# Kernel tuning notes

Measured on AMD Instinct MI355X. Metric: run time of the kernel, lower is better.

Reference implementation:

```python
import jax, jax.numpy as jnp
import numpy as np
import math

EMBED_DIMS = 256
NUM_LANDMARKS = 40  # hard-coded k=40 in the original module
B, N = 2, 8192


def setup_inputs() -> dict:
    key = jax.random.key(0)
    ks = jax.random.split(key, 9)
    C = EMBED_DIMS
    w = lambda k: jax.random.normal(k, (C, C), dtype=jnp.float32) * 0.02
    b = lambda k: jax.random.normal(k, (C,), dtype=jnp.float32) * 0.02
    return {
        "query": jax.random.normal(ks[0], (B, N, C), dtype=jnp.float32),
        "Wq": w(ks[1]), "bq": b(ks[2]),
        "Wk": w(ks[3]), "bk": b(ks[4]),
        "Wv": w(ks[5]), "bv": b(ks[6]),
        "Wo": w(ks[7]), "bo": b(ks[8]),
    }


def reference(query, Wq, bq, Wk, bk, Wv, bv, Wo, bo):
    # key = value = identity = query (defaults in the original forward)
    C = query.shape[-1]
    scaling = math.sqrt(C)

    q = query @ Wq.T + bq  # [B, N, C]
    k = query @ Wk.T + bk
    v = query @ Wv.T + bv

    # Full similarity only to score keys: score_m[b, m] = sum_n sim_nm[b, n, m]
    sim_nm = jnp.einsum('bnc,bmc->bnm', q, k) / scaling  # [B, N, N]
    score_m = sim_nm.sum(axis=1)                          # [B, N]

    _, top_idx = jax.lax.top_k(score_m, NUM_LANDMARKS)    # [B, 40]
    selected = jnp.take_along_axis(k, top_idx[:, :, None], axis=1)  # [B, 40, C]

    sim_qn = jax.nn.softmax(jnp.einsum('bnc,bkc->bnk', q, selected) / scaling, axis=-1)  # [B, N, 40]
    sim_km = jax.nn.softmax(jnp.einsum('bmc,bkc->bmk', k, selected) / scaling, axis=-1)  # [B, N, 40]

    sim_qk = jnp.einsum('bnk,bmk->bnm', sim_qn, sim_km)   # [B, N, N]
    out = jnp.einsum('bnm,bmc->bnc', sim_qk, v)           # [B, N, C]
    out = out @ Wo.T + bo
    return query + out  # identity residual; dropouts are identity at p=0
```

## Files before the change

### kernel.cpp

```cpp
#include <hip/hip_runtime.h>
#include <cstddef>
#include <cstdint>

#define BATCH 2
#define SEQ 8192
#define CH 256
#define NLM 40
#define MROWS (BATCH * SEQ)
#define INV_SCALE 0.0625f
#define NCBLK 256

typedef unsigned short ushort_t;
typedef __attribute__((ext_vector_type(8))) short short8;
typedef __attribute__((ext_vector_type(4))) float floatx4;

__device__ __forceinline__ ushort_t f2bf(float f) {
    unsigned int u = __float_as_uint(f);
    u += 0x7FFFu + ((u >> 16) & 1u);
    return (ushort_t)(u >> 16);
}
__device__ __forceinline__ float bf2f(ushort_t u) {
    return __uint_as_float(((unsigned)u) << 16);
}

__global__ __launch_bounds__(256) void convert_colsum(const float* __restrict__ x,
                                                      ushort_t* __restrict__ xbf,
                                                      float* __restrict__ partial) {
    __shared__ float red[4][256];
    const int b = blockIdx.y;
    const int r0 = blockIdx.x * 32;
    const int t = threadIdx.x;
    const int c4 = (t & 63) * 4;
    const int rg = t >> 6;
    const float* base = x + ((size_t)b * SEQ + r0) * 256;
    ushort_t* obase = xbf + ((size_t)b * SEQ + r0) * 256;
    float4 s = {0.f, 0.f, 0.f, 0.f};
#pragma unroll
    for (int i = 0; i < 8; i++) {
        const int r = rg + i * 4;
        const float4 a = *(const float4*)&base[(size_t)r * 256 + c4];
        uint2 o;
        o.x = f2bf(a.x) | ((unsigned)f2bf(a.y) << 16);
        o.y = f2bf(a.z) | ((unsigned)f2bf(a.w) << 16);
        *(uint2*)&obase[(size_t)r * 256 + c4] = o;
        s.x += a.x; s.y += a.y; s.z += a.z; s.w += a.w;
    }
    *(float4*)&red[rg][c4] = s;
    __syncthreads();
    const float tot = red[0][t] + red[1][t] + red[2][t] + red[3][t];
    partial[((size_t)b * NCBLK + blockIdx.x) * 256 + t] = tot;
}

__global__ __launch_bounds__(1024) void ws_kernel(const float* __restrict__ partial,
                                                  const float* __restrict__ Wq,
                                                  const float* __restrict__ bq,
                                                  const float* __restrict__ Wk,
                                                  float* __restrict__ ws,
                                                  float* __restrict__ tmat) {
    const int b = blockIdx.x;
    __shared__ float xs[256];
    __shared__ float qs[256];
    __shared__ float ppart[4][256];
    const int t = threadIdx.x;
    {
        float* tz = tmat + (size_t)b * NLM * 256;
        for (int i = t; i < NLM * 256; i += 1024) tz[i] = 0.f;
    }
    {
        const int c = t & 255, qd = t >> 8;
        const float* pb = partial + ((size_t)b * NCBLK + qd * 64) * 256 + c;
        float a = 0.f;
#pragma unroll 8
        for (int i = 0; i < 64; i++) a += pb[(size_t)i * 256];
        ppart[qd][c] = a;
    }
    __syncthreads();
    if (t < 256) xs[t] = ppart[0][t] + ppart[1][t] + ppart[2][t] + ppart[3][t];
    __syncthreads();
    const int lane = t & 63, w = t >> 6;
    for (int g = 0; g < 16; g++) {
        const int o = w * 16 + g;
        const float4 wq = *(const float4*)&Wq[(size_t)o * 256 + lane * 4];
        const float4 x4 = *(const float4*)&xs[lane * 4];
        float d = wq.x * x4.x + wq.y * x4.y + wq.z * x4.z + wq.w * x4.w;
#pragma unroll
        for (int off = 32; off >= 1; off >>= 1) d += __shfl_down(d, off);
        if (lane == 0) qs[o] = d + 8192.0f * bq[o];
    }
    __syncthreads();
    const int c = t & 255, part = t >> 8;
    float a = 0.f;
    for (int o = part * 64; o < part * 64 + 64; o++)
        a += Wk[(size_t)o * 256 + c] * qs[o];
    ppart[part][c] = a;
    __syncthreads();
    if (t < 256)
        ws[b * 256 + t] = ppart[0][t] + ppart[1][t] + ppart[2][t] + ppart[3][t];
}

__global__ __launch_bounds__(256) void gemm_qkv_score(const ushort_t* __restrict__ xbf,
                                                      const float* __restrict__ Wq,
                                                      const float* __restrict__ Wk,
                                                      const float* __restrict__ Wv,
                                                      const float* __restrict__ bq,
                                                      const float* __restrict__ bk,
                                                      const float* __restrict__ bv,
                                                      ushort_t* __restrict__ qkv,
                                                      const float* __restrict__ query,
                                                      const float* __restrict__ ws,
                                                      float* __restrict__ score) {
    __shared__ __align__(16) ushort_t As[128 * 72];
    __shared__ __align__(16) ushort_t Bs[64 * 40];
    const int z = blockIdx.z;
    const int t = threadIdx.x;
    const int lane = t & 63;
    const int w = t >> 6;

    if (z == 3) {
        const int blk = blockIdx.y * 4 + blockIdx.x;
#pragma unroll
        for (int i = 0; i < 8; i++) {
            const int g = blk * 32 + i * 4 + w;
            const int b = g >> 13;
            const int m = g & 8191;
            const float4 kv = *(const float4*)&query[(size_t)g * 256 + lane * 4];
            const float4 qs = *(const float4*)&ws[b * 256 + lane * 4];
            float d = kv.x * qs.x + kv.y * qs.y + kv.z * qs.z + kv.w * qs.w;
#pragma unroll
            for (int off = 32; off >= 1; off >>= 1) d += __shfl_down(d, off);
            if (lane == 0) score[(size_t)b * SEQ + m] = d * INV_SCALE;
        }
        return;
    }

    const float* __restrict__ W = (z == 0) ? Wq : (z == 1) ? Wk : Wv;
    const float* __restrict__ bias = (z == 0) ? bq : (z == 1) ? bk : bv;
    ushort_t* __restrict__ out = qkv + (size_t)z * MROWS * 256;
    const int o0 = blockIdx.x * 64;
    const int m0 = blockIdx.y * 128;
    const int quad = lane >> 4;
    const int l16 = lane & 15;

    floatx4 acc[2][4];
#pragma unroll
    for (int rt = 0; rt < 2; rt++)
#pragma unroll
        for (int ct = 0; ct < 4; ct++) acc[rt][ct] = (floatx4){0.f, 0.f, 0.f, 0.f};

    for (int kc = 0; kc < 256; kc += 32) {
#pragma unroll
        for (int u = 0; u < 2; u++) {
            const int cid = t + u * 256;
            const int row = cid >> 2, off = cid & 3;
            *(uint4*)&As[row * 40 + off * 8] =
                *(const uint4*)&xbf[(size_t)(m0 + row) * 256 + kc + off * 8];
        }
        {
            const int row = t >> 2, off = t & 3;
            const float* wp = &W[(size_t)(o0 + row) * 256 + kc + off * 8];
            const float4 a = *(const float4*)wp;
            const float4 c = *(const float4*)(wp + 4);
            uint4 o;
            o.x = f2bf(a.x) | ((unsigned)f2bf(a.y) << 16);
            o.y = f2bf(a.z) | ((unsigned)f2bf(a.w) << 16);
            o.z = f2bf(c.x) | ((unsigned)f2bf(c.y) << 16);
            o.w = f2bf(c.z) | ((unsigned)f2bf(c.w) << 16);
            *(uint4*)&Bs[row * 40 + off * 8] = o;
        }
        __syncthreads();
        short8 a[2], b[4];
#pragma unroll
        for (int rt = 0; rt < 2; rt++)
            a[rt] = *(const short8*)&As[(w * 32 + rt * 16 + l16) * 40 + quad * 8];
#pragma unroll
        for (int ct = 0; ct < 4; ct++)
            b[ct] = *(const short8*)&Bs[(ct * 16 + l16) * 40 + quad * 8];
#pragma unroll
        for (int rt = 0; rt < 2; rt++)
#pragma unroll
            for (int ct = 0; ct < 4; ct++)
                acc[rt][ct] = __builtin_amdgcn_mfma_f32_16x16x32_bf16(
                    a[rt], b[ct], acc[rt][ct], 0, 0, 0);
        __syncthreads();
    }

#pragma unroll
    for (int rt = 0; rt < 2; rt++) {
#pragma unroll
        for (int ct = 0; ct < 4; ct++) {
            const int col = ct * 16 + l16;
            const float bb = bias[o0 + col];
#pragma unroll
            for (int reg = 0; reg < 4; reg++) {
                const int row = w * 32 + rt * 16 + quad * 4 + reg;
                As[row * 72 + col] = f2bf(acc[rt][ct][reg] + bb);
            }
        }
    }
    __syncthreads();
#pragma unroll
    for (int u = 0; u < 4; u++) {
        const int cid = t + u * 256;
        const int row = cid >> 3;
        const int off = (cid & 7) * 8;
        *(uint4*)&out[(size_t)(m0 + row) * 256 + o0 + off] =
            *(const uint4*)&As[row * 72 + off];
    }
}

__global__ __launch_bounds__(1024) void topk_gather(const float* __restrict__ score,
                                                    const ushort_t* __restrict__ kmat,
                                                    float* __restrict__ sel) {
    const int b = blockIdx.x;
    const int t = threadIdx.x;
    __shared__ unsigned hist[256];
    __shared__ unsigned wsum[64];
    __shared__ unsigned sPrefix, sMask, sRem, sNeq;
    __shared__ int sNgt;
    __shared__ int top[NLM];
    __shared__ unsigned topkey[NLM];

    unsigned key[8];
#pragma unroll
    for (int j = 0; j < 8; j++) {
        const unsigned u = __float_as_uint(score[(size_t)b * SEQ + t + j * 1024]);
        key[j] = u ^ (unsigned)(((int)u >> 31) | 0x80000000);
    }
    if (t == 0) { sPrefix = 0; sMask = 0; sRem = NLM; sNgt = 0; sNeq = 0; }

    for (int lvl = 0; lvl < 4; lvl++) {
        const int shift = 24 - 8 * lvl;
        if (t < 256) hist[t] = 0;
        __syncthreads();
        const unsigned pfx = sPrefix, msk = sMask;
#pragma unroll
        for (int j = 0; j < 8; j++)
            if (((key[j] ^ pfx) & msk) == 0)
                atomicAdd(&hist[(key[j] >> shift) & 255u], 1u);
        __syncthreads();
        if (t < 64) wsum[t] = hist[t * 4] + hist[t * 4 + 1] + hist[t * 4 + 2] + hist[t * 4 + 3];
        __syncthreads();
        if (t == 0) {
            unsigned rem = sRem, cum = 0;
            int g = 63;
            for (; g > 0; g--) { if (cum + wsum[g] >= rem) break; cum += wsum[g]; }
            int d = g * 4 + 3;
            for (; d > g * 4; d--) { if (cum + hist[d] >= rem) break; cum += hist[d]; }
            sRem = rem - cum;
            sPrefix |= ((unsigned)d) << shift;
            sMask |= 255u << shift;
        }
        __syncthreads();
    }
    const unsigned K40 = sPrefix;
    const unsigned rem = sRem;
    const int ngt = NLM - (int)rem;

#pragma unroll
    for (int j = 0; j < 8; j++) {
        if (key[j] > K40) {
            const int slot = atomicAdd(&sNgt, 1);
            top[slot] = t + j * 1024; topkey[slot] = key[j];
        } else if (key[j] == K40) {
            const unsigned e = atomicAdd(&sNeq, 1u);
            if (e < rem) {
                const int slot = ngt + (int)e;
                top[slot] = t + j * 1024; topkey[slot] = key[j];
            }
        }
    }
    __syncthreads();

    if (t < 64) {
        unsigned long long c = (t < NLM)
            ? ((((unsigned long long)(~topkey[t])) << 32) | (unsigned)top[t])
            : 0xFFFFFFFFFFFFFFFFull;
#pragma unroll
        for (int kk = 2; kk <= 64; kk <<= 1) {
#pragma unroll
            for (int j = kk >> 1; j >= 1; j >>= 1) {
                const unsigned long long o = __shfl_xor(c, j);
                const bool takeMin = ((t & kk) == 0) == ((t & j) == 0);
                const bool less = c < o;
                c = (takeMin == less) ? c : o;
            }
        }
        if (t < NLM) top[t] = (int)(c & 0xFFFFFFFFu);
    }
    __syncthreads();

    for (int f = t; f < NLM * 256; f += 1024) {
        const int j = f >> 8;
        const int cc = f & 255;
        sel[(size_t)b * SEQ * 0 + (size_t)b * NLM * 256 + f] = bf2f(kmat[((size_t)b * SEQ + top[j]) * 256 + cc]);
    }
}

__global__ __launch_bounds__(256, 4) void sim_fused(const ushort_t* __restrict__ qbf,
                                                    const ushort_t* __restrict__ kbf,
                                                    const ushort_t* __restrict__ vbf,
                                                    const float* __restrict__ sel,
                                                    float* __restrict__ simq,
                                                    float* __restrict__ tmat) {
    __shared__ __align__(16) char smem[43008];
    float (*As_)[68] = (float(*)[68])smem;
    float (*St_)[68] = (float(*)[68])(smem + 17408);
    float (*Ps)[40]  = (float(*)[40])smem;
    ushort_t* Vs     = (ushort_t*)(smem + 10240);
    const int b = blockIdx.y;
    const int n0 = blockIdx.x * 64;
    const int t = threadIdx.x;
    const int r = t >> 2, c = t & 3;
    const ushort_t* __restrict__ A = (blockIdx.z == 0) ? qbf : kbf;
    const ushort_t* __restrict__ Arow = A + ((size_t)b * SEQ + n0) * 256;
    const float* __restrict__ Sb = sel + (size_t)b * NLM * 256;

    float acc[10];
#pragma unroll
    for (int j = 0; j < 10; j++) acc[j] = 0.f;

    for (int kc = 0; kc < 256; kc += 64) {
#pragma unroll
        for (int u = 0; u < 4; u++) {
            const int f = t + u * 256;
            const int row = f >> 4;
            const int c4 = (f & 15) * 4;
            const uint2 raw = *(const uint2*)&Arow[(size_t)row * 256 + kc + c4];
            float4 fa;
            fa.x = __uint_as_float((raw.x & 0xFFFFu) << 16);
            fa.y = __uint_as_float(raw.x & 0xFFFF0000u);
            fa.z = __uint_as_float((raw.y & 0xFFFFu) << 16);
            fa.w = __uint_as_float(raw.y & 0xFFFF0000u);
            *(float4*)&As_[row][c4] = fa;
        }
#pragma unroll
        for (int u = 0; u < 3; u++) {
            const int f = t + u * 256;
            if (f < 640) {
                const int row = f >> 4;
                const int c4 = (f & 15) * 4;
                *(float4*)&St_[row][c4] = *(const float4*)&Sb[(size_t)row * 256 + kc + c4];
            }
        }
        __syncthreads();
#pragma unroll 1
        for (int i = 0; i < 64; i += 4) {
            const float4 a = *(const float4*)&As_[r][i];
#pragma unroll
            for (int j = 0; j < 10; j++) {
                const float4 s = *(const float4*)&St_[c * 10 + j][i];
                acc[j] = fmaf(a.x, s.x, acc[j]);
                acc[j] = fmaf(a.y, s.y, acc[j]);
                acc[j] = fmaf(a.z, s.z, acc[j]);
                acc[j] = fmaf(a.w, s.w, acc[j]);
            }
        }
        __syncthreads();
    }

    float mx = -1e30f;
#pragma unroll
    for (int j = 0; j < 10; j++) {
        acc[j] *= INV_SCALE;
        mx = fmaxf(mx, acc[j]);
    }
    mx = fmaxf(mx, __shfl_xor(mx, 1));
    mx = fmaxf(mx, __shfl_xor(mx, 2));
    float sum = 0.f;
#pragma unroll
    for (int j = 0; j < 10; j++) {
        acc[j] = expf(acc[j] - mx);
        sum += acc[j];
    }
    sum += __shfl_xor(sum, 1);
    sum += __shfl_xor(sum, 2);
    const float inv = 1.f / sum;
#pragma unroll
    for (int j = 0; j < 10; j++) acc[j] *= inv;

    if (blockIdx.z == 0) {
        float* __restrict__ dst = &simq[((size_t)b * SEQ + n0 + r) * NLM + c * 10];
#pragma unroll
        for (int j2 = 0; j2 < 5; j2++) {
            float2 o; o.x = acc[2 * j2]; o.y = acc[2 * j2 + 1];
            *(float2*)&dst[2 * j2] = o;
        }
        return;
    }

#pragma unroll
    for (int j = 0; j < 10; j++) Ps[r][c * 10 + j] = acc[j];
#pragma unroll
    for (int u = 0; u < 8; u++) {
        const int cid = t + u * 256;
        const int row = cid >> 5, off = (cid & 31) * 8;
        *(uint4*)&Vs[row * 256 + off] =
            *(const uint4*)&vbf[((size_t)b * SEQ + n0 + row) * 256 + off];
    }
    __syncthreads();

    float tac[40];
#pragma unroll
    for (int j = 0; j < 40; j++) tac[j] = 0.f;

#pragma unroll 2
    for (int m = 0; m < 64; m++) {
        const float vv = bf2f(Vs[m * 256 + t]);
#pragma unroll
        for (int j4 = 0; j4 < 10; j4++) {
            const float4 p = *(const float4*)&Ps[m][j4 * 4];
            tac[j4 * 4 + 0] = fmaf(p.x, vv, tac[j4 * 4 + 0]);
            tac[j4 * 4 + 1] = fmaf(p.y, vv, tac[j4 * 4 + 1]);
            tac[j4 * 4 + 2] = fmaf(p.z, vv, tac[j4 * 4 + 2]);
            tac[j4 * 4 + 3] = fmaf(p.w, vv, tac[j4 * 4 + 3]);
        }
    }
#pragma unroll
    for (int j = 0; j < 40; j++)
        atomicAdd(&tmat[(size_t)b * NLM * 256 + j * 256 + t], tac[j]);
}

__global__ __launch_bounds__(256) void out_pre_kernel(const float* __restrict__ simq,
                                                      const float* __restrict__ tmat,
                                                      ushort_t* __restrict__ outp_bf) {
    __shared__ float Pm[64][40];
    const int g0 = blockIdx.x * 64;
    const int b = g0 >> 13;
    const int t = threadIdx.x;
    float* pflat = &Pm[0][0];
    for (int f = t; f < 64 * NLM; f += 256) pflat[f] = simq[(size_t)g0 * NLM + f];
    float tc[40];
#pragma unroll
    for (int l = 0; l < 40; l++) tc[l] = tmat[(size_t)b * NLM * 256 + l * 256 + t];
    __syncthreads();
#pragma unroll 2
    for (int m = 0; m < 64; m++) {
        float a = 0.f;
#pragma unroll
        for (int j4 = 0; j4 < 10; j4++) {
            const float4 p = *(const float4*)&Pm[m][j4 * 4];
            a = fmaf(p.x, tc[j4 * 4 + 0], a);
            a = fmaf(p.y, tc[j4 * 4 + 1], a);
            a = fmaf(p.z, tc[j4 * 4 + 2], a);
            a = fmaf(p.w, tc[j4 * 4 + 3], a);
        }
        outp_bf[((size_t)g0 + m) * 256 + t] = f2bf(a);
    }
}

__global__ __launch_bounds__(256) void gemm_out(const ushort_t* __restrict__ Abf,
                                                const float* __restrict__ Wo,
                                                const float* __restrict__ bias,
                                                const float* __restrict__ resid,
                                                float* __restrict__ out) {
    __shared__ __align__(16) char smem[128 * 68 * 4];
    ushort_t* As = (ushort_t*)smem;
    ushort_t* Bs = (ushort_t*)(smem + 128 * 40 * 2);
    float* Ft = (float*)smem;
    const int t = threadIdx.x;
    const int o0 = blockIdx.x * 64;
    const int m0 = blockIdx.y * 128;
    const int lane = t & 63;
    const int w = t >> 6;
    const int quad = lane >> 4;
    const int l16 = lane & 15;

    floatx4 acc[2][4];
#pragma unroll
    for (int rt = 0; rt < 2; rt++)
#pragma unroll
        for (int ct = 0; ct < 4; ct++) acc[rt][ct] = (floatx4){0.f, 0.f, 0.f, 0.f};

    for (int kc = 0; kc < 256; kc += 32) {
#pragma unroll
        for (int u = 0; u < 2; u++) {
            const int cid = t + u * 256;
            const int row = cid >> 2, off = cid & 3;
            *(uint4*)&As[row * 40 + off * 8] =
                *(const uint4*)&Abf[(size_t)(m0 + row) * 256 + kc + off * 8];
        }
        {
            const int row = t >> 2, off = t & 3;
            const float* wp = &Wo[(size_t)(o0 + row) * 256 + kc + off * 8];
            const float4 a = *(const float4*)wp;
            const float4 c = *(const float4*)(wp + 4);
            uint4 o;
            o.x = f2bf(a.x) | ((unsigned)f2bf(a.y) << 16);
            o.y = f2bf(a.z) | ((unsigned)f2bf(a.w) << 16);
            o.z = f2bf(c.x) | ((unsigned)f2bf(c.y) << 16);
            o.w = f2bf(c.z) | ((unsigned)f2bf(c.w) << 16);
            *(uint4*)&Bs[row * 40 + off * 8] = o;
        }
        __syncthreads();
        short8 a[2], b[4];
#pragma unroll
        for (int rt = 0; rt < 2; rt++)
            a[rt] = *(const short8*)&As[(w * 32 + rt * 16 + l16) * 40 + quad * 8];
#pragma unroll
        for (int ct = 0; ct < 4; ct++)
            b[ct] = *(const short8*)&Bs[(ct * 16 + l16) * 40 + quad * 8];
#pragma unroll
        for (int rt = 0; rt < 2; rt++)
#pragma unroll
            for (int ct = 0; ct < 4; ct++)
                acc[rt][ct] = __builtin_amdgcn_mfma_f32_16x16x32_bf16(
                    a[rt], b[ct], acc[rt][ct], 0, 0, 0);
        __syncthreads();
    }

#pragma unroll
    for (int rt = 0; rt < 2; rt++) {
#pragma unroll
        for (int ct = 0; ct < 4; ct++) {
            const int col = ct * 16 + l16;
            const float bb = bias[o0 + col];
#pragma unroll
            for (int reg = 0; reg < 4; reg++) {
                const int row = w * 32 + rt * 16 + quad * 4 + reg;
                Ft[row * 68 + col] = acc[rt][ct][reg] + bb;
            }
        }
    }
    __syncthreads();
#pragma unroll
    for (int u = 0; u < 8; u++) {
        const int cid = t + u * 256;
        const int row = cid >> 4;
        const int off = (cid & 15) * 4;
        const float4 v = *(const float4*)&Ft[row * 68 + off];
        const float4 r4 = *(const float4*)&resid[(size_t)(m0 + row) * 256 + o0 + off];
        float4 o;
        o.x = v.x + r4.x; o.y = v.y + r4.y; o.z = v.z + r4.z; o.w = v.w + r4.w;
        *(float4*)&out[(size_t)(m0 + row) * 256 + o0 + off] = o;
    }
}

extern "C" void kernel_launch(void* const* d_in, const int* in_sizes, int n_in,
                              void* d_out, int out_size, void* d_ws, size_t ws_size,
                              hipStream_t stream) {
    const float* query = (const float*)d_in[0];
    const float* Wq = (const float*)d_in[1];
    const float* bq = (const float*)d_in[2];
    const float* Wk = (const float*)d_in[3];
    const float* bk = (const float*)d_in[4];
    const float* Wv = (const float*)d_in[5];
    const float* bv = (const float*)d_in[6];
    const float* Wo = (const float*)d_in[7];
    const float* bo = (const float*)d_in[8];
    float* out = (float*)d_out;

    char* p = (char*)d_ws;
    float* simq  = (float*)p;            p += (size_t)MROWS * NLM * 4;
    float* sel   = (float*)p;            p += (size_t)BATCH * NLM * 256 * 4;
    float* tmat  = (float*)p;            p += (size_t)BATCH * NLM * 256 * 4;
    float* partial = (float*)p;          p += (size_t)BATCH * NCBLK * 256 * 4;
    float* ws    = (float*)p;            p += (size_t)BATCH * 256 * 4;
    float* score = (float*)p;            p += (size_t)BATCH * SEQ * 4;
    ushort_t* qkv = (ushort_t*)p;        p += (size_t)3 * MROWS * 256 * 2;
    ushort_t* xbf = (ushort_t*)p;        p += (size_t)MROWS * 256 * 2;
    ushort_t* qbf = qkv;
    ushort_t* kbf = qkv + (size_t)MROWS * 256;
    ushort_t* vbf = qkv + (size_t)2 * MROWS * 256;
    ushort_t* outp_bf = xbf;

    const dim3 blk(256);

    convert_colsum<<<dim3(SEQ / 32, BATCH), blk, 0, stream>>>(query, xbf, partial);
    ws_kernel<<<dim3(BATCH), dim3(1024), 0, stream>>>(partial, Wq, bq, Wk, ws, tmat);

    gemm_qkv_score<<<dim3(4, MROWS / 128, 4), blk, 0, stream>>>(
        xbf, Wq, Wk, Wv, bq, bk, bv, qkv, query, ws, score);

    topk_gather<<<dim3(BATCH), dim3(1024), 0, stream>>>(score, kbf, sel);

    sim_fused<<<dim3(SEQ / 64, BATCH, 2), blk, 0, stream>>>(qbf, kbf, vbf, sel, simq, tmat);

    out_pre_kernel<<<dim3(MROWS / 64), blk, 0, stream>>>(simq, tmat, outp_bf);
    gemm_out<<<dim3(4, MROWS / 128), blk, 0, stream>>>(outp_bf, Wo, bo, query, out);
}
```

Measured before the change: 204.7 us.

## Fold Wo into landmark matrix and convert query to bf16 inside QKV GEMM

The output projection is reassociated: tmat (40x256 per batch) is multiplied by Wo once in a small tw_kernel, so out_final computes simq·TW + bias + residual directly. This removes the bf16 intermediate write and the full 16384x256x256 output GEMM. Separately, the bf16 copy of query is no longer materialised; the QKV GEMM converts fp32 query tiles on load, and the colsum kernel only reduces. The trade-off is reading fp32 query several times in the GEMM (once per output-column block and z), and a serial tw_kernel with only 8 blocks.

```diff
diff --git a/kernel.cpp b/kernel.cpp
--- a/kernel.cpp
+++ b/kernel.cpp
@@ -23,9 +23,8 @@
     return __uint_as_float(((unsigned)u) << 16);
 }
 
-__global__ __launch_bounds__(256) void convert_colsum(const float* __restrict__ x,
-                                                      ushort_t* __restrict__ xbf,
-                                                      float* __restrict__ partial) {
+__global__ __launch_bounds__(256) void colsum_kernel(const float* __restrict__ x,
+                                                     float* __restrict__ partial) {
     __shared__ float red[4][256];
     const int b = blockIdx.y;
     const int r0 = blockIdx.x * 32;
@@ -33,16 +32,11 @@
     const int c4 = (t & 63) * 4;
     const int rg = t >> 6;
     const float* base = x + ((size_t)b * SEQ + r0) * 256;
-    ushort_t* obase = xbf + ((size_t)b * SEQ + r0) * 256;
     float4 s = {0.f, 0.f, 0.f, 0.f};
 #pragma unroll
     for (int i = 0; i < 8; i++) {
         const int r = rg + i * 4;
         const float4 a = *(const float4*)&base[(size_t)r * 256 + c4];
-        uint2 o;
-        o.x = f2bf(a.x) | ((unsigned)f2bf(a.y) << 16);
-        o.y = f2bf(a.z) | ((unsigned)f2bf(a.w) << 16);
-        *(uint2*)&obase[(size_t)r * 256 + c4] = o;
         s.x += a.x; s.y += a.y; s.z += a.z; s.w += a.w;
     }
     *(float4*)&red[rg][c4] = s;
@@ -98,7 +92,7 @@
         ws[b * 256 + t] = ppart[0][t] + ppart[1][t] + ppart[2][t] + ppart[3][t];
 }
 
-__global__ __launch_bounds__(256) void gemm_qkv_score(const ushort_t* __restrict__ xbf,
+__global__ __launch_bounds__(256) void gemm_qkv_score(const float* __restrict__ query,
                                                       const float* __restrict__ Wq,
                                                       const float* __restrict__ Wk,
                                                       const float* __restrict__ Wv,
@@ -106,7 +100,6 @@
                                                       const float* __restrict__ bk,
                                                       const float* __restrict__ bv,
                                                       ushort_t* __restrict__ qkv,
-                                                      const float* __restrict__ query,
                                                       const float* __restrict__ ws,
                                                       float* __restrict__ score) {
     __shared__ __align__(16) ushort_t As[128 * 72];
@@ -152,8 +145,15 @@
         for (int u = 0; u < 2; u++) {
             const int cid = t + u * 256;
             const int row = cid >> 2, off = cid & 3;
-            *(uint4*)&As[row * 40 + off * 8] =
-                *(const uint4*)&xbf[(size_t)(m0 + row) * 256 + kc + off * 8];
+            const float* xp = &query[(size_t)(m0 + row) * 256 + kc + off * 8];
+            const float4 a = *(const float4*)xp;
+            const float4 c = *(const float4*)(xp + 4);
+            uint4 o;
+            o.x = f2bf(a.x) | ((unsigned)f2bf(a.y) << 16);
+            o.y = f2bf(a.z) | ((unsigned)f2bf(a.w) << 16);
+            o.z = f2bf(c.x) | ((unsigned)f2bf(c.y) << 16);
+            o.w = f2bf(c.z) | ((unsigned)f2bf(c.w) << 16);
+            *(uint4*)&As[row * 40 + off * 8] = o;
         }
         {
             const int row = t >> 2, off = t & 3;
@@ -292,7 +292,7 @@
     for (int f = t; f < NLM * 256; f += 1024) {
         const int j = f >> 8;
         const int cc = f & 255;
-        sel[(size_t)b * SEQ * 0 + (size_t)b * NLM * 256 + f] = bf2f(kmat[((size_t)b * SEQ + top[j]) * 256 + cc]);
+        sel[(size_t)b * NLM * 256 + f] = bf2f(kmat[((size_t)b * SEQ + top[j]) * 256 + cc]);
     }
 }
 
@@ -420,9 +420,38 @@
         atomicAdd(&tmat[(size_t)b * NLM * 256 + j * 256 + t], tac[j]);
 }
 
-__global__ __launch_bounds__(256) void out_pre_kernel(const float* __restrict__ simq,
-                                                      const float* __restrict__ tmat,
-                                                      ushort_t* __restrict__ outp_bf) {
+__global__ __launch_bounds__(256) void tw_kernel(const float* __restrict__ tmat,
+                                                 const float* __restrict__ Wo,
+                                                 float* __restrict__ TW) {
+    __shared__ float Ps[10][256];
+    const int b = blockIdx.y;
+    const int lg = blockIdx.x;
+    const int t = threadIdx.x;
+    float* pflat = &Ps[0][0];
+    for (int f = t; f < 10 * 256; f += 256)
+        pflat[f] = tmat[(size_t)b * NLM * 256 + lg * 10 * 256 + f];
+    __syncthreads();
+
+    float tw[10];
+#pragma unroll
+    for (int j = 0; j < 10; j++) tw[j] = 0.f;
+    const float* __restrict__ wrow = &Wo[(size_t)t * 256];
+#pragma unroll 4
+    for (int o = 0; o < 256; o++) {
+        const float wo = wrow[o];
+#pragma unroll
+        for (int j = 0; j < 10; j++) tw[j] = fmaf(Ps[j][o], wo, tw[j]);
+    }
+#pragma unroll
+    for (int j = 0; j < 10; j++)
+        TW[(size_t)b * NLM * 256 + (lg * 10 + j) * 256 + t] = tw[j];
+}
+
+__global__ __launch_bounds__(256) void out_final(const float* __restrict__ simq,
+                                                 const float* __restrict__ TW,
+                                                 const float* __restrict__ bo,
+                                                 const float* __restrict__ resid,
+                                                 float* __restrict__ out) {
     __shared__ float Pm[64][40];
     const int g0 = blockIdx.x * 64;
     const int b = g0 >> 13;
@@ -431,8 +460,9 @@
     for (int f = t; f < 64 * NLM; f += 256) pflat[f] = simq[(size_t)g0 * NLM + f];
     float tc[40];
 #pragma unroll
-    for (int l = 0; l < 40; l++) tc[l] = tmat[(size_t)b * NLM * 256 + l * 256 + t];
-    __syncthreads();
+    for (int l = 0; l < 40; l++) tc[l] = TW[(size_t)b * NLM * 256 + l * 256 + t];
+    __syncthreads();
+    const float bb = bo[t];
 #pragma unroll 2
     for (int m = 0; m < 64; m++) {
         float a = 0.f;
@@ -444,94 +474,8 @@
             a = fmaf(p.z, tc[j4 * 4 + 2], a);
             a = fmaf(p.w, tc[j4 * 4 + 3], a);
         }
-        outp_bf[((size_t)g0 + m) * 256 + t] = f2bf(a);
-    }
-}
-
-__global__ __launch_bounds__(256) void gemm_out(const ushort_t* __restrict__ Abf,
-                                                const float* __restrict__ Wo,
-                                                const float* __restrict__ bias,
-                                                const float* __restrict__ resid,
-                                                float* __restrict__ out) {
-    __shared__ __align__(16) char smem[128 * 68 * 4];
-    ushort_t* As = (ushort_t*)smem;
-    ushort_t* Bs = (ushort_t*)(smem + 128 * 40 * 2);
-    float* Ft = (float*)smem;
-    const int t = threadIdx.x;
-    const int o0 = blockIdx.x * 64;
-    const int m0 = blockIdx.y * 128;
-    const int lane = t & 63;
-    const int w = t >> 6;
-    const int quad = lane >> 4;
-    const int l16 = lane & 15;
-
-    floatx4 acc[2][4];
-#pragma unroll
-    for (int rt = 0; rt < 2; rt++)
-#pragma unroll
-        for (int ct = 0; ct < 4; ct++) acc[rt][ct] = (floatx4){0.f, 0.f, 0.f, 0.f};
-
-    for (int kc = 0; kc < 256; kc += 32) {
-#pragma unroll
-        for (int u = 0; u < 2; u++) {
-            const int cid = t + u * 256;
-            const int row = cid >> 2, off = cid & 3;
-            *(uint4*)&As[row * 40 + off * 8] =
-                *(const uint4*)&Abf[(size_t)(m0 + row) * 256 + kc + off * 8];
-        }
-        {
-            const int row = t >> 2, off = t & 3;
-            const float* wp = &Wo[(size_t)(o0 + row) * 256 + kc + off * 8];
-            const float4 a = *(const float4*)wp;
-            const float4 c = *(const float4*)(wp + 4);
-            uint4 o;
-            o.x = f2bf(a.x) | ((unsigned)f2bf(a.y) << 16);
-            o.y = f2bf(a.z) | ((unsigned)f2bf(a.w) << 16);
-            o.z = f2bf(c.x) | ((unsigned)f2bf(c.y) << 16);
-            o.w = f2bf(c.z) | ((unsigned)f2bf(c.w) << 16);
-            *(uint4*)&Bs[row * 40 + off * 8] = o;
-        }
-        __syncthreads();
-        short8 a[2], b[4];
-#pragma unroll
-        for (int rt = 0; rt < 2; rt++)
-            a[rt] = *(const short8*)&As[(w * 32 + rt * 16 + l16) * 40 + quad * 8];
-#pragma unroll
-        for (int ct = 0; ct < 4; ct++)
-            b[ct] = *(const short8*)&Bs[(ct * 16 + l16) * 40 + quad * 8];
-#pragma unroll
-        for (int rt = 0; rt < 2; rt++)
-#pragma unroll
-            for (int ct = 0; ct < 4; ct++)
-                acc[rt][ct] = __builtin_amdgcn_mfma_f32_16x16x32_bf16(
-                    a[rt], b[ct], acc[rt][ct], 0, 0, 0);
-        __syncthreads();
-    }
-
-#pragma unroll
-    for (int rt = 0; rt < 2; rt++) {
-#pragma unroll
-        for (int ct = 0; ct < 4; ct++) {
-            const int col = ct * 16 + l16;
-            const float bb = bias[o0 + col];
-#pragma unroll
-            for (int reg = 0; reg < 4; reg++) {
-                const int row = w * 32 + rt * 16 + quad * 4 + reg;
-                Ft[row * 68 + col] = acc[rt][ct][reg] + bb;
-            }
-        }
-    }
-    __syncthreads();
-#pragma unroll
-    for (int u = 0; u < 8; u++) {
-        const int cid = t + u * 256;
-        const int row = cid >> 4;
-        const int off = (cid & 15) * 4;
-        const float4 v = *(const float4*)&Ft[row * 68 + off];
-        const float4 r4 = *(const float4*)&resid[(size_t)(m0 + row) * 256 + o0 + off];
-        float4 o;
-        o.x = v.x + r4.x; o.y = v.y + r4.y; o.z = v.z + r4.z; o.w = v.w + r4.w;
-        *(float4*)&out[(size_t)(m0 + row) * 256 + o0 + off] = o;
+        out[((size_t)g0 + m) * 256 + t] =
+            a + bb + resid[((size_t)g0 + m) * 256 + t];
     }
 }
 
@@ -553,28 +497,27 @@
     float* simq  = (float*)p;            p += (size_t)MROWS * NLM * 4;
     float* sel   = (float*)p;            p += (size_t)BATCH * NLM * 256 * 4;
     float* tmat  = (float*)p;            p += (size_t)BATCH * NLM * 256 * 4;
+    float* TW    = (float*)p;            p += (size_t)BATCH * NLM * 256 * 4;
     float* partial = (float*)p;          p += (size_t)BATCH * NCBLK * 256 * 4;
     float* ws    = (float*)p;            p += (size_t)BATCH * 256 * 4;
     float* score = (float*)p;            p += (size_t)BATCH * SEQ * 4;
     ushort_t* qkv = (ushort_t*)p;        p += (size_t)3 * MROWS * 256 * 2;
-    ushort_t* xbf = (ushort_t*)p;        p += (size_t)MROWS * 256 * 2;
     ushort_t* qbf = qkv;
     ushort_t* kbf = qkv + (size_t)MROWS * 256;
     ushort_t* vbf = qkv + (size_t)2 * MROWS * 256;
-    ushort_t* outp_bf = xbf;
 
     const dim3 blk(256);
 
-    convert_colsum<<<dim3(SEQ / 32, BATCH), blk, 0, stream>>>(query, xbf, partial);
+    colsum_kernel<<<dim3(SEQ / 32, BATCH), blk, 0, stream>>>(query, partial);
     ws_kernel<<<dim3(BATCH), dim3(1024), 0, stream>>>(partial, Wq, bq, Wk, ws, tmat);
 
     gemm_qkv_score<<<dim3(4, MROWS / 128, 4), blk, 0, stream>>>(
-        xbf, Wq, Wk, Wv, bq, bk, bv, qkv, query, ws, score);
+        query, Wq, Wk, Wv, bq, bk, bv, qkv, ws, score);
 
     topk_gather<<<dim3(BATCH), dim3(1024), 0, stream>>>(score, kbf, sel);
 
     sim_fused<<<dim3(SEQ / 64, BATCH, 2), blk, 0, stream>>>(qbf, kbf, vbf, sel, simq, tmat);
 
-    out_pre_kernel<<<dim3(MROWS / 64), blk, 0, stream>>>(simq, tmat, outp_bf);
-    gemm_out<<<dim3(4, MROWS / 128), blk, 0, stream>>>(outp_bf, Wo, bo, query, out);
-}
+    tw_kernel<<<dim3(4, BATCH), blk, 0, stream>>>(tmat, Wo, TW);
+    out_final<<<dim3(MROWS / 64), blk, 0, stream>>>(simq, TW, bo, query, out);
+}
```

Result: slower. 215.9 us (+5.5%).
